# Kernel tuning notes

Measured on AMD Instinct MI355X. Metric: run time of the kernel, lower is better.

Reference implementation:

```python
import jax, jax.numpy as jnp
import numpy as np

DIM = 16      # latent_dim == sec
SEC = 16
SUB = 16      # sub_sec
E = SEC * SUB # num_elements = 256
TH = 0.2
BATCH = 128
SL = BATCH // 2
TAU = 0.0001

bexpm = jax.vmap(jax.scipy.linalg.expm)


def _commut(ge):
    # commutative(div=dim): loop over K=E//DIM block pairs with cumulative block
    # swaps; loss = sum_k cumsum(per-pair sq-diff)[k] / (DIM*E)^2
    K = E // DIM
    basis = ge.reshape(DIM, DIM * E)                 # [d, d*E]
    bm = jnp.matmul(ge, basis).reshape(DIM * E, DIM * E)
    R = bm[:K * DIM, :K * DIM].reshape(K, DIM, K, DIM)
    c = 2.0 * ((R - jnp.transpose(R, (2, 1, 0, 3))) ** 2).sum((1, 3))  # [K,K]
    iu, ju = np.triu_indices(K, k=1)                 # lexicographic pair order
    return jnp.cumsum(c[iu, ju]).sum() / float((DIM * E) ** 2)


def _independent(z, ge, sec_idx):
    B = z.shape[0]
    syms = bexpm(ge)                                 # [E,d,d]
    diff = z - jnp.matmul(z, syms)                   # [E,B,d]
    d2 = (diff ** 2).reshape(-1, DIM)
    sparse = jnp.mean((d2.sum(-1) - d2.max(-1)) ** 2)
    par = diff.reshape(SEC, SUB * B, DIM)            # [SEC,M,d]
    nrm = jnp.linalg.norm(par, axis=-1, keepdims=True)
    nn_ = jnp.einsum('smi,sni->smn', nrm, nrm)       # [SEC,M,M]
    dd = jnp.einsum('smd,snd->smn', par, par)
    parallel = jnp.mean(-jnp.log((dd / nn_) ** 2 + 1e-9))
    sel = diff.reshape(SEC, SUB, B, DIM)[jnp.arange(SEC), sec_idx]
    sel = sel.reshape(SEC * B, DIM)
    sn = jnp.linalg.norm(sel, axis=-1, keepdims=True)
    ratio = (sel @ sel.T) / (sn @ sn.T)
    mask = jnp.asarray(1.0 - np.kron(np.eye(SEC, dtype=np.float32),
                                     np.ones((B, B), np.float32)))
    orth = jnp.mean((ratio ** 2) * mask)
    return orth, parallel, _commut(ge), sparse


def reference(mean, logvar, latent_z, group_elements, lin_w, lin_b,
              gumbel_noise, sec_idx):
    B = latent_z.shape[0]
    sl = B // 2
    mean1, mean2 = mean[:sl], mean[sl:]
    std1 = jnp.exp(0.5 * logvar[:sl])
    std2 = jnp.exp(0.5 * mean[sl:])   # (faithful to source bug: uses mean)
    z1, z2 = latent_z[:sl], latent_z[sl:]
    orth, parallel, commut, sparse = _independent(latent_z, group_elements, sec_idx)

    zd = z1 - z2
    target = (jnp.abs(zd) > TH).astype(jnp.int32).reshape(-1)   # [sl*SEC]
    feat = jnp.concatenate([mean1, std1, mean2, std2], -1)       # [sl,4d]
    prob = feat @ lin_w.T + lin_b                                # [sl,18*SEC]
    sector_logits = prob[:, :2 * SEC].reshape(-1, 2)             # [sl*SEC,2]
    p = jax.nn.softmax(sector_logits, -1)
    ls = jax.nn.log_softmax(p, -1)    # cross_entropy applied to softmax output
    sector_loss = -jnp.take_along_axis(ls, target[:, None], 1).sum() / sl

    attn = jax.nn.softmax((sector_logits + gumbel_noise) / TAU, -1)
    switch = jnp.where((attn[:, 0] >= 0.5) | (attn[:, 1] > 0.5), attn[:, 1], 0.0)
    switch = switch.reshape(sl, SEC)
    fprob = jax.nn.softmax(prob[:, 2 * SEC:].reshape(sl, SEC, SUB), -1)
    fprob = fprob.reshape(sl, E)
    w = jnp.repeat(switch, SUB, axis=-1) * fprob                 # [sl,E]
    syms = w[:, :, None, None] * group_elements[None]            # [sl,E,d,d]
    sub_syms = syms.reshape(sl, SEC, SUB, DIM, DIM).sum(2)       # [sl,SEC,d,d]
    S = syms.sum(1)                                              # [sl,d,d]
    fwd_syms = bexpm(S)
    inv_syms = bexpm(-S)
    attn_score = jnp.concatenate([switch, fprob], -1)            # [sl,SEC+E]

    tz1 = jnp.einsum('bd,bde->be', z1, fwd_syms)
    tz2 = jnp.einsum('bd,bde->be', z2, inv_syms)
    equivariant = jnp.mean((tz2 - z1) ** 2) + jnp.mean((tz1 - z2) ** 2)
    return (tz1, tz2, fwd_syms, equivariant, attn_score,
            orth, parallel, commut, sparse, sector_loss, sub_syms)


def setup_inputs() -> dict:
    key = jax.random.key(0)
    ks = jax.random.split(key, 7)
    mean = jax.random.normal(ks[0], (BATCH, DIM), jnp.float32)
    logvar = jax.random.normal(ks[1], (BATCH, DIM), jnp.float32)
    latent_z = jax.random.normal(ks[2], (BATCH, DIM), jnp.float32)
    group_elements = 0.1 * jax.random.normal(ks[3], (E, DIM, DIM), jnp.float32)
    lin_w = 0.1 * jax.random.normal(ks[4], ((SUB + 2) * SEC, 4 * DIM), jnp.float32)
    lin_b = jnp.zeros(((SUB + 2) * SEC,), jnp.float32)
    u = jax.random.uniform(ks[5], (SL * SEC, 2), jnp.float32, 1e-6, 1.0 - 1e-6)
    gumbel_noise = -jnp.log(-jnp.log(u))
    sec_idx = jax.random.randint(ks[6], (SEC,), 0, SEC, jnp.int32)
    return {'mean': mean, 'logvar': logvar, 'latent_z': latent_z,
            'group_elements': group_elements, 'lin_w': lin_w, 'lin_b': lin_b,
            'gumbel_noise': gumbel_noise, 'sec_idx': sec_idx}
```

## Files before the change

kernel.cpp:

```cpp
#include <hip/hip_runtime.h>
#include <math.h>

#define O_TZ1      0
#define O_TZ2      1024
#define O_FWD      2048
#define O_EQUI     18432
#define O_ATTN     18433
#define O_ORTH     35841
#define O_PAR      35842
#define O_COMM     35843
#define O_SPARSE   35844
#define O_SECLOSS  35845
#define O_SUB      35846

#define P_SECLOSS  0
#define P_SPARSE   64
#define P_CPAIR    320
#define P_EQUI     440
#define P_PAR      504
#define P_ORTH     2680

typedef short s16x8 __attribute__((ext_vector_type(8)));
typedef float f32x4 __attribute__((ext_vector_type(4)));

__device__ __forceinline__ void block_store(float v, float* red, int t, float* slot, float scale)
{
    red[t] = v;
    __syncthreads();
    for (int off = 128; off > 0; off >>= 1) { if (t < off) red[t] += red[t+off]; __syncthreads(); }
    if (t == 0) *slot = red[0] * scale;
}

__device__ __forceinline__ unsigned short f2bf(float x)
{
    unsigned int u = __float_as_uint(x);
    u = (u + 0x7FFFu + ((u >> 16) & 1u)) >> 16;
    return (unsigned short)u;
}

__device__ __forceinline__ void expm_core(const float* __restrict__ src, float sign,
                                          float* sm, int* shi, int t)
{
    float* As = sm; float* T = sm + 256; float* P = sm + 512; float* rowsum = sm + 768;
    float a = src[t];
    As[t] = a;
    __syncthreads();
    if (t < 16) {
        float rs = 0.f;
        #pragma unroll
        for (int k = 0; k < 16; ++k) rs += fabsf(As[t*16+k]);
        rowsum[t] = rs;
    }
    __syncthreads();
    if (t == 0) {
        float nrm = 0.f;
        for (int i = 0; i < 16; ++i) nrm = fmaxf(nrm, rowsum[i]);
        int s = 0;
        if (nrm > 0.66f) { s = (int)ceilf(log2f(nrm * 1.51515f)); if (s < 0) s = 0; }
        *shi = s;
    }
    __syncthreads();
    int sq = *shi;
    float scale = sign * exp2f((float)(-sq));
    int i = t >> 4, j = t & 15;
    float as = a * scale;
    As[t] = as;
    T[t]  = ((i==j) ? 1.0f : 0.0f) + as;
    P[t]  = as;
    __syncthreads();
    for (int k = 2; k <= 8; ++k) {
        float accv = 0.f;
        #pragma unroll
        for (int m = 0; m < 16; ++m) accv += P[i*16+m]*As[m*16+j];
        float rk = 1.0f/(float)k;
        __syncthreads();
        float term = accv * rk;
        P[t] = term;
        T[t] += term;
        __syncthreads();
    }
    for (int q = 0; q < sq; ++q) {
        float accv = 0.f;
        #pragma unroll
        for (int m = 0; m < 16; ++m) accv += T[i*16+m]*T[m*16+j];
        __syncthreads();
        T[t] = accv;
        __syncthreads();
    }
}

template <bool DO_LOG>
__device__ __forceinline__ float gram_mfma(const unsigned short* __restrict__ diffb,
                                           int baseM, int baseN, int t)
{
    int lane = t & 63;
    int wave = t >> 6;
    int quad = lane >> 4;
    int col  = lane & 15;
    const s16x8* pb = (const s16x8*)diffb;
    s16x8 zf = {0,0,0,0,0,0,0,0};
    s16x8 A0 = zf, A1 = zf;
    s16x8 B0 = zf, B1 = zf, B2 = zf, B3 = zf, B4 = zf, B5 = zf, B6 = zf, B7 = zf;
    if (quad < 2) {
        int q = quad;
        A0 = pb[(baseM + wave*32      + col)*2 + q];
        A1 = pb[(baseM + wave*32 + 16 + col)*2 + q];
        B0 = pb[(baseN +   0 + col)*2 + q];
        B1 = pb[(baseN +  16 + col)*2 + q];
        B2 = pb[(baseN +  32 + col)*2 + q];
        B3 = pb[(baseN +  48 + col)*2 + q];
        B4 = pb[(baseN +  64 + col)*2 + q];
        B5 = pb[(baseN +  80 + col)*2 + q];
        B6 = pb[(baseN +  96 + col)*2 + q];
        B7 = pb[(baseN + 112 + col)*2 + q];
    }
    f32x4 cz = {0.f, 0.f, 0.f, 0.f};
    float accf = 0.f;
#define GTILE(AF, BF) { \
    f32x4 c = __builtin_amdgcn_mfma_f32_16x16x32_bf16(AF, BF, cz, 0, 0, 0); \
    _Pragma("unroll") \
    for (int r_ = 0; r_ < 4; ++r_) { \
        float v_ = c[r_]; \
        float x_ = v_*v_ + 1e-9f; \
        accf += DO_LOG ? __log2f(x_) : x_; \
    } }
    GTILE(A0,B0) GTILE(A0,B1) GTILE(A0,B2) GTILE(A0,B3)
    GTILE(A0,B4) GTILE(A0,B5) GTILE(A0,B6) GTILE(A0,B7)
    GTILE(A1,B0) GTILE(A1,B1) GTILE(A1,B2) GTILE(A1,B3)
    GTILE(A1,B4) GTILE(A1,B5) GTILE(A1,B6) GTILE(A1,B7)
#undef GTILE
    return accf;
}

__global__ void k_stage1(const float* __restrict__ mean, const float* __restrict__ logvar,
                         const float* __restrict__ latent, const float* __restrict__ ge,
                         const float* __restrict__ lin_w, const float* __restrict__ lin_b,
                         const float* __restrict__ gumbel,
                         float* __restrict__ out, float* __restrict__ S_ws,
                         unsigned short* __restrict__ diffb, float* __restrict__ part)
{
    __shared__ float smem[4864];
    __shared__ int shi;
    int bid = blockIdx.x;
    int t = threadIdx.x;

    if (bid < 64) {
        int b = bid;
        float* feat = smem;
        float* probb = smem + 64;
        float* red16 = smem + 352;
        float* wrow = smem + 368;
        if (t < 64) {
            int k = t; float v;
            if (k < 16)       v = mean[b*16 + k];
            else if (k < 32)  v = expf(0.5f * logvar[b*16 + (k-16)]);
            else if (k < 48)  v = mean[(64+b)*16 + (k-32)];
            else              v = expf(0.5f * mean[(64+b)*16 + (k-48)]);
            feat[k] = v;
        }
        __syncthreads();
        for (int j = t; j < 288; j += 256) {
            float a = lin_b[j];
            const float* wr = lin_w + j*64;
            #pragma unroll
            for (int k = 0; k < 64; ++k) a += feat[k]*wr[k];
            probb[j] = a;
        }
        __syncthreads();
        if (t < 16) {
            int s = t;
            float l0 = probb[2*s], l1 = probb[2*s+1];
            float M = fmaxf(l0,l1);
            float e0 = expf(l0-M), e1 = expf(l1-M);
            float Z = e0+e1;
            float p0 = e0/Z, p1 = e1/Z;
            float M2 = fmaxf(p0,p1);
            float lse = M2 + logf(expf(p0-M2)+expf(p1-M2));
            float ls0 = p0 - lse, ls1 = p1 - lse;
            float z1v = latent[b*16+s], z2v = latent[(64+b)*16+s];
            int tt = (fabsf(z1v - z2v) > 0.2f) ? 1 : 0;
            red16[s] = -(tt ? ls1 : ls0);
            int r = b*16 + s;
            float x0 = (l0 + gumbel[2*r])   * 10000.0f;
            float x1 = (l1 + gumbel[2*r+1]) * 10000.0f;
            float Ma = fmaxf(x0,x1);
            float a0 = expf(x0-Ma), a1 = expf(x1-Ma);
            float Za = a0+a1;
            a0 /= Za; a1 /= Za;
            float sw = ((a0 >= 0.5f) || (a1 > 0.5f)) ? a1 : 0.0f;
            out[O_ATTN + b*272 + s] = sw;
            const float* fl = &probb[32 + s*16];
            float mf = fl[0];
            #pragma unroll
            for (int u = 1; u < 16; ++u) mf = fmaxf(mf, fl[u]);
            float ex[16]; float Zf = 0.f;
            #pragma unroll
            for (int u = 0; u < 16; ++u) { ex[u] = expf(fl[u]-mf); Zf += ex[u]; }
            float rZ = 1.0f/Zf;
            #pragma unroll
            for (int u = 0; u < 16; ++u) {
                float fp = ex[u]*rZ;
                out[O_ATTN + b*272 + 16 + s*16 + u] = fp;
                wrow[s*16 + u] = sw*fp;
            }
        }
        __syncthreads();
        if (t == 0) {
            float s = 0.f;
            for (int i = 0; i < 16; ++i) s += red16[i];
            part[P_SECLOSS + b] = s;
        }
        float Stot = 0.f;
        for (int s = 0; s < 16; ++s) {
            float a = 0.f;
            #pragma unroll
            for (int u = 0; u < 16; ++u)
                a += wrow[s*16+u] * ge[(s*16+u)*256 + t];
            out[O_SUB + b*4096 + s*256 + t] = a;
            Stot += a;
        }
        S_ws[b*256 + t] = Stot;
    } else if (bid < 320) {
        int e = bid - 64;
        float* zsh = smem + 784;
        float* red = smem + 2832;
        #pragma unroll
        for (int q = 0; q < 8; ++q) zsh[t+256*q] = latent[t+256*q];
        expm_core(ge + e*256, 1.0f, smem, &shi, t);
        const float* T = smem + 256;
        float pv = 0.f;
        if (t < 128) {
            float zr[16];
            #pragma unroll
            for (int k = 0; k < 16; ++k) zr[k] = zsh[t*16+k];
            float dv[16];
            float sum = 0.f, mx = 0.f;
            #pragma unroll
            for (int d = 0; d < 16; ++d) {
                float a = 0.f;
                #pragma unroll
                for (int k = 0; k < 16; ++k) a += zr[k]*T[k*16+d];
                float v = zr[d] - a;
                dv[d] = v;
                float v2 = v*v;
                sum += v2; mx = fmaxf(mx, v2);
            }
            float sm2 = sum - mx;
            pv = sm2*sm2;
            float ri = 1.0f / sqrtf(sum);
            unsigned int pk[8];
            #pragma unroll
            for (int d = 0; d < 8; ++d) {
                unsigned short h0 = f2bf(dv[2*d]   * ri);
                unsigned short h1 = f2bf(dv[2*d+1] * ri);
                pk[d] = (unsigned int)h0 | ((unsigned int)h1 << 16);
            }
            uint4* dst = (uint4*)(diffb + (size_t)(e*128 + t)*16);
            dst[0] = make_uint4(pk[0], pk[1], pk[2], pk[3]);
            dst[1] = make_uint4(pk[4], pk[5], pk[6], pk[7]);
        }
        block_store(pv, red, t, part + P_SPARSE + e, 1.0f);
    } else {
        int idx = bid - 320;
        float* G = smem;
        float* gA = smem + 4096;
        float* gB = smem + 4352;
        float* red = smem + 4608;
        int a2 = 0, cnt = 15, rem = idx;
        while (rem >= cnt) { rem -= cnt; a2++; cnt--; }
        int b2 = a2 + 1 + rem;
        #pragma unroll
        for (int q = 0; q < 16; ++q) {
            int ii = t + 256*q;
            int k = ii >> 8, x = ii & 255;
            G[ii] = ge[k*16*256 + x];
        }
        gA[t] = ge[a2*256+t];
        gB[t] = ge[b2*256+t];
        __syncthreads();
        int i = t >> 4, j = t & 15;
        float v1 = 0.f, v2 = 0.f;
        #pragma unroll
        for (int k = 0; k < 16; ++k) {
            v1 += gA[i*16+k]*G[k*256 + b2*16 + j];
            v2 += gB[i*16+k]*G[k*256 + a2*16 + j];
        }
        float d = v1 - v2;
        block_store(d*d, red, t, part + P_CPAIR + idx, 2.0f);
    }
}

__global__ void __launch_bounds__(256) k_stage2(const float* __restrict__ latent,
                                                const float* __restrict__ S_ws,
                                                const unsigned short* __restrict__ diffb,
                                                const int* __restrict__ sec_idx,
                                                float* __restrict__ out,
                                                float* __restrict__ part)
{
    __shared__ float smem[1040];
    __shared__ int shi;
    int bid = blockIdx.x;
    int t = threadIdx.x;
    float* red = smem + 784;

    if (bid < 64) {
        int b = bid;
        expm_core(S_ws + b*256, 1.0f, smem, &shi, t);
        const float* T = smem + 256;
        out[O_FWD + b*256 + t] = T[t];
        float t1 = 0.f, z1d = 0.f, z2d = 0.f;
        if (t < 16) {
            int d = t;
            #pragma unroll
            for (int k = 0; k < 16; ++k) t1 += latent[b*16+k] * T[k*16+d];
            out[O_TZ1 + b*16 + d] = t1;
            z1d = latent[b*16+d];
            z2d = latent[(64+b)*16+d];
        }
        expm_core(S_ws + b*256, -1.0f, smem, &shi, t);
        float t2 = 0.f, ep = 0.f;
        if (t < 16) {
            int d = t;
            #pragma unroll
            for (int k = 0; k < 16; ++k) t2 += latent[(64+b)*16+k] * T[k*16+d];
            out[O_TZ2 + b*16 + d] = t2;
            ep = (t2 - z1d)*(t2 - z1d) + (t1 - z2d)*(t1 - z2d);
        }
        block_store(ep, red, t, part + P_EQUI + b, 1.0f);
    } else if (bid < 2240) {
        int tile = bid - 64;
        int s = tile & 15;
        int r = tile >> 4;
        int tm = 0;
        while (r >= 16 - tm) { r -= 16 - tm; tm++; }
        int tn = tm + r;
        float accf = gram_mfma<true>(diffb, s*2048 + tm*128, s*2048 + tn*128, t);
        float wt = (tm == tn) ? 1.0f : 2.0f;
        block_store(accf, red, t, part + P_PAR + tile, wt);
    } else {
        int idx = bid - 2240;
        int sm = 0, cnt = 15, rem = idx;
        while (rem >= cnt) { rem -= cnt; sm++; cnt--; }
        int sn = sm + 1 + rem;
        int em = sm*16 + sec_idx[sm];
        int en = sn*16 + sec_idx[sn];
        float accf = gram_mfma<false>(diffb, em*128, en*128, t);
        block_store(accf, red, t, part + P_ORTH + idx, 2.0f);
    }
}

__global__ void k_final(const float* __restrict__ part, float* __restrict__ out)
{
    __shared__ double dred[256];
    int t = threadIdx.x;

    double local = 0.0;
    for (int i = t; i < 2176; i += 256) local += (double)part[P_PAR + i];
    dred[t] = local;
    __syncthreads();
    for (int off = 128; off > 0; off >>= 1) { if (t < off) dred[t] += dred[t+off]; __syncthreads(); }
    double s_par = dred[0];
    __syncthreads();

    local = 0.0;
    if (t < 120) local += (double)part[P_ORTH + t];
    dred[t] = local;
    __syncthreads();
    for (int off = 128; off > 0; off >>= 1) { if (t < off) dred[t] += dred[t+off]; __syncthreads(); }
    double s_orth = dred[0];
    __syncthreads();

    local = 0.0;
    if (t < 64) local += (double)part[P_EQUI + t];
    if (t < 64) local += 0.0;
    dred[t] = local;
    __syncthreads();
    for (int off = 128; off > 0; off >>= 1) { if (t < off) dred[t] += dred[t+off]; __syncthreads(); }
    double s_equi = dred[0];
    __syncthreads();

    local = (t < 64) ? (double)part[P_SECLOSS + t] : 0.0;
    dred[t] = local;
    __syncthreads();
    for (int off = 128; off > 0; off >>= 1) { if (t < off) dred[t] += dred[t+off]; __syncthreads(); }
    double s_sec = dred[0];
    __syncthreads();

    dred[t] = (double)part[P_SPARSE + t];
    __syncthreads();
    for (int off = 128; off > 0; off >>= 1) { if (t < off) dred[t] += dred[t+off]; __syncthreads(); }
    double s_spa = dred[0];
    __syncthreads();

    local = 0.0;
    if (t < 120) local = (double)(120 - t) * (double)part[P_CPAIR + t];
    dred[t] = local;
    __syncthreads();
    for (int off = 128; off > 0; off >>= 1) { if (t < off) dred[t] += dred[t+off]; __syncthreads(); }

    if (t == 0) {
        out[O_COMM]    = (float)(dred[0] / 16777216.0);
        out[O_EQUI]    = (float)(s_equi / 1024.0);
        out[O_ORTH]    = (float)(s_orth / (2048.0*2048.0));
        out[O_PAR]     = (float)(-s_par * 0.6931471805599453 / 67108864.0);
        out[O_SPARSE]  = (float)(s_spa / 32768.0);
        out[O_SECLOSS] = (float)(s_sec / 64.0);
    }
}

extern "C" void kernel_launch(void* const* d_in, const int* in_sizes, int n_in,
                              void* d_out, int out_size, void* d_ws, size_t ws_size,
                              hipStream_t stream)
{
    const float* mean    = (const float*)d_in[0];
    const float* logvar  = (const float*)d_in[1];
    const float* latent  = (const float*)d_in[2];
    const float* ge      = (const float*)d_in[3];
    const float* lin_w   = (const float*)d_in[4];
    const float* lin_b   = (const float*)d_in[5];
    const float* gumbel  = (const float*)d_in[6];
    const int*   sec_idx = (const int*)d_in[7];
    float* out = (float*)d_out;

    char* ws = (char*)d_ws;
    float* part = (float*)ws;
    float* S_ws = (float*)(ws + 16384);
    unsigned short* diffb = (unsigned short*)(ws + 81920);

    k_stage1<<<440,  256, 0, stream>>>(mean, logvar, latent, ge, lin_w, lin_b, gumbel,
                                       out, S_ws, diffb, part);
    k_stage2<<<2360, 256, 0, stream>>>(latent, S_ws, diffb, sec_idx, out, part);
    k_final <<<1,    256, 0, stream>>>(part, out);
}
```

Baseline: 94.46 us.

## Fuse final reduction into stage2 via atomic accumulators and last-block finish

Removes the separate single-block final kernel. Stage2 blocks now add their partial sums into double-precision global accumulators with atomics and bump an arrival counter, and the last block to arrive computes and writes the scalar losses. The log-sum in the gram tiles is also restructured to multiply four terms and take one log2 instead of four. This saves a kernel launch and its serialization at the cost of atomics on contended addresses. The product-then-log form could lose precision or underflow when values are tiny.

```diff
diff --git a/kernel.cpp b/kernel.cpp
--- a/kernel.cpp
+++ b/kernel.cpp
@@ -16,9 +16,8 @@
 #define P_SECLOSS  0
 #define P_SPARSE   64
 #define P_CPAIR    320
-#define P_EQUI     440
-#define P_PAR      504
-#define P_ORTH     2680
+
+#define S2_BLOCKS  2360u
 
 typedef short s16x8 __attribute__((ext_vector_type(8)));
 typedef float f32x4 __attribute__((ext_vector_type(4)));
@@ -29,6 +28,22 @@
     __syncthreads();
     for (int off = 128; off > 0; off >>= 1) { if (t < off) red[t] += red[t+off]; __syncthreads(); }
     if (t == 0) *slot = red[0] * scale;
+}
+
+__device__ __forceinline__ bool block_arrive(float v, float* red, int t, double* dst, float scale,
+                                             unsigned int* counter, unsigned int* lf)
+{
+    red[t] = v;
+    __syncthreads();
+    for (int off = 128; off > 0; off >>= 1) { if (t < off) red[t] += red[t+off]; __syncthreads(); }
+    if (t == 0) {
+        double oldv = atomicAdd(dst, (double)(red[0] * scale));
+        float dep = (float)oldv;
+        __asm__ volatile("" : : "v"(dep));
+        *lf = (atomicAdd(counter, 1u) == S2_BLOCKS - 1u) ? 1u : 0u;
+    }
+    __syncthreads();
+    return *lf != 0u;
 }
 
 __device__ __forceinline__ unsigned short f2bf(float x)
@@ -118,11 +133,12 @@
     float accf = 0.f;
 #define GTILE(AF, BF) { \
     f32x4 c = __builtin_amdgcn_mfma_f32_16x16x32_bf16(AF, BF, cz, 0, 0, 0); \
-    _Pragma("unroll") \
-    for (int r_ = 0; r_ < 4; ++r_) { \
-        float v_ = c[r_]; \
-        float x_ = v_*v_ + 1e-9f; \
-        accf += DO_LOG ? __log2f(x_) : x_; \
+    if (DO_LOG) { \
+        float p0 = (c[0]*c[0] + 1e-9f) * (c[1]*c[1] + 1e-9f); \
+        float p1 = (c[2]*c[2] + 1e-9f) * (c[3]*c[3] + 1e-9f); \
+        accf += __log2f(p0 * p1); \
+    } else { \
+        accf += c[0]*c[0] + c[1]*c[1] + c[2]*c[2] + c[3]*c[3]; \
     } }
     GTILE(A0,B0) GTILE(A0,B1) GTILE(A0,B2) GTILE(A0,B3)
     GTILE(A0,B4) GTILE(A0,B5) GTILE(A0,B6) GTILE(A0,B7)
@@ -132,17 +148,35 @@
     return accf;
 }
 
+__device__ __forceinline__ double dsum(const float* __restrict__ p, int n, int t, double* dred)
+{
+    double local = 0.0;
+    for (int i = t; i < n; i += 256) local += (double)p[i];
+    dred[t] = local;
+    __syncthreads();
+    for (int off = 128; off > 0; off >>= 1) { if (t < off) dred[t] += dred[t+off]; __syncthreads(); }
+    double r = dred[0];
+    __syncthreads();
+    return r;
+}
+
 __global__ void k_stage1(const float* __restrict__ mean, const float* __restrict__ logvar,
                          const float* __restrict__ latent, const float* __restrict__ ge,
                          const float* __restrict__ lin_w, const float* __restrict__ lin_b,
                          const float* __restrict__ gumbel,
                          float* __restrict__ out, float* __restrict__ S_ws,
-                         unsigned short* __restrict__ diffb, float* __restrict__ part)
+                         unsigned short* __restrict__ diffb, float* __restrict__ part,
+                         double* __restrict__ acc, unsigned int* __restrict__ counter)
 {
     __shared__ float smem[4864];
     __shared__ int shi;
     int bid = blockIdx.x;
     int t = threadIdx.x;
+
+    if (bid == 0 && t == 0) {
+        acc[0] = 0.0; acc[1] = 0.0; acc[2] = 0.0;
+        *counter = 0u;
+    }
 
     if (bid < 64) {
         int b = bid;
@@ -295,13 +329,19 @@
                                                 const unsigned short* __restrict__ diffb,
                                                 const int* __restrict__ sec_idx,
                                                 float* __restrict__ out,
-                                                float* __restrict__ part)
+                                                float* __restrict__ part,
+                                                double* __restrict__ acc,
+                                                unsigned int* __restrict__ counter)
 {
     __shared__ float smem[1040];
+    __shared__ double dred[256];
+    __shared__ double sacc[3];
     __shared__ int shi;
+    __shared__ unsigned int lf;
     int bid = blockIdx.x;
     int t = threadIdx.x;
     float* red = smem + 784;
+    bool last;
 
     if (bid < 64) {
         int b = bid;
@@ -326,7 +366,7 @@
             out[O_TZ2 + b*16 + d] = t2;
             ep = (t2 - z1d)*(t2 - z1d) + (t1 - z2d)*(t1 - z2d);
         }
-        block_store(ep, red, t, part + P_EQUI + b, 1.0f);
+        last = block_arrive(ep, red, t, &acc[2], 1.0f, counter, &lf);
     } else if (bid < 2240) {
         int tile = bid - 64;
         int s = tile & 15;
@@ -336,7 +376,7 @@
         int tn = tm + r;
         float accf = gram_mfma<true>(diffb, s*2048 + tm*128, s*2048 + tn*128, t);
         float wt = (tm == tn) ? 1.0f : 2.0f;
-        block_store(accf, red, t, part + P_PAR + tile, wt);
+        last = block_arrive(accf, red, t, &acc[0], wt, counter, &lf);
     } else {
         int idx = bid - 2240;
         int sm = 0, cnt = 15, rem = idx;
@@ -345,66 +385,31 @@
         int em = sm*16 + sec_idx[sm];
         int en = sn*16 + sec_idx[sn];
         float accf = gram_mfma<false>(diffb, em*128, en*128, t);
-        block_store(accf, red, t, part + P_ORTH + idx, 2.0f);
-    }
-}
-
-__global__ void k_final(const float* __restrict__ part, float* __restrict__ out)
-{
-    __shared__ double dred[256];
-    int t = threadIdx.x;
-
-    double local = 0.0;
-    for (int i = t; i < 2176; i += 256) local += (double)part[P_PAR + i];
-    dred[t] = local;
-    __syncthreads();
-    for (int off = 128; off > 0; off >>= 1) { if (t < off) dred[t] += dred[t+off]; __syncthreads(); }
-    double s_par = dred[0];
-    __syncthreads();
-
-    local = 0.0;
-    if (t < 120) local += (double)part[P_ORTH + t];
-    dred[t] = local;
-    __syncthreads();
-    for (int off = 128; off > 0; off >>= 1) { if (t < off) dred[t] += dred[t+off]; __syncthreads(); }
-    double s_orth = dred[0];
-    __syncthreads();
-
-    local = 0.0;
-    if (t < 64) local += (double)part[P_EQUI + t];
-    if (t < 64) local += 0.0;
-    dred[t] = local;
-    __syncthreads();
-    for (int off = 128; off > 0; off >>= 1) { if (t < off) dred[t] += dred[t+off]; __syncthreads(); }
-    double s_equi = dred[0];
-    __syncthreads();
-
-    local = (t < 64) ? (double)part[P_SECLOSS + t] : 0.0;
-    dred[t] = local;
-    __syncthreads();
-    for (int off = 128; off > 0; off >>= 1) { if (t < off) dred[t] += dred[t+off]; __syncthreads(); }
-    double s_sec = dred[0];
-    __syncthreads();
-
-    dred[t] = (double)part[P_SPARSE + t];
-    __syncthreads();
-    for (int off = 128; off > 0; off >>= 1) { if (t < off) dred[t] += dred[t+off]; __syncthreads(); }
-    double s_spa = dred[0];
-    __syncthreads();
-
-    local = 0.0;
-    if (t < 120) local = (double)(120 - t) * (double)part[P_CPAIR + t];
-    dred[t] = local;
-    __syncthreads();
-    for (int off = 128; off > 0; off >>= 1) { if (t < off) dred[t] += dred[t+off]; __syncthreads(); }
-
-    if (t == 0) {
-        out[O_COMM]    = (float)(dred[0] / 16777216.0);
-        out[O_EQUI]    = (float)(s_equi / 1024.0);
-        out[O_ORTH]    = (float)(s_orth / (2048.0*2048.0));
-        out[O_PAR]     = (float)(-s_par * 0.6931471805599453 / 67108864.0);
-        out[O_SPARSE]  = (float)(s_spa / 32768.0);
-        out[O_SECLOSS] = (float)(s_sec / 64.0);
+        last = block_arrive(accf, red, t, &acc[1], 2.0f, counter, &lf);
+    }
+
+    if (last) {
+        if (t == 0) {
+            sacc[0] = atomicAdd(&acc[0], 0.0);
+            sacc[1] = atomicAdd(&acc[1], 0.0);
+            sacc[2] = atomicAdd(&acc[2], 0.0);
+        }
+        __syncthreads();
+        double s_sec = dsum(part + P_SECLOSS, 64, t, dred);
+        double s_spa = dsum(part + P_SPARSE, 256, t, dred);
+        double local = 0.0;
+        if (t < 120) local = (double)(120 - t) * (double)part[P_CPAIR + t];
+        dred[t] = local;
+        __syncthreads();
+        for (int off = 128; off > 0; off >>= 1) { if (t < off) dred[t] += dred[t+off]; __syncthreads(); }
+        if (t == 0) {
+            out[O_COMM]    = (float)(dred[0] / 16777216.0);
+            out[O_EQUI]    = (float)(sacc[2] / 1024.0);
+            out[O_ORTH]    = (float)(sacc[1] / (2048.0*2048.0));
+            out[O_PAR]     = (float)(-sacc[0] * 0.6931471805599453 / 67108864.0);
+            out[O_SPARSE]  = (float)(s_spa / 32768.0);
+            out[O_SECLOSS] = (float)(s_sec / 64.0);
+        }
     }
 }
 
@@ -423,12 +428,13 @@
     float* out = (float*)d_out;
 
     char* ws = (char*)d_ws;
-    float* part = (float*)ws;
+    double* acc = (double*)ws;
+    float* part = (float*)(ws + 64);
+    unsigned int* counter = (unsigned int*)(ws + 12288);
     float* S_ws = (float*)(ws + 16384);
     unsigned short* diffb = (unsigned short*)(ws + 81920);
 
     k_stage1<<<440,  256, 0, stream>>>(mean, logvar, latent, ge, lin_w, lin_b, gumbel,
-                                       out, S_ws, diffb, part);
-    k_stage2<<<2360, 256, 0, stream>>>(latent, S_ws, diffb, sec_idx, out, part);
-    k_final <<<1,    256, 0, stream>>>(part, out);
-}
+                                       out, S_ws, diffb, part, acc, counter);
+    k_stage2<<<2360, 256, 0, stream>>>(latent, S_ws, diffb, sec_idx, out, part, acc, counter);
+}
```

Result: slower. 117.2 us (+24.1%).

## Stage gram tiles through LDS, batch log2 calls, use wave-shuffle reductions

Applied to the files above, without the earlier changes.

The gram-tile blocks in stage2 now copy their 128+128 bf16 rows into padded shared memory with coalesced 16-byte loads. MFMA operands are then read from LDS instead of issuing scattered global loads per wave. The log-sum now multiplies four squared terms before one log2, cutting transcendental count, at some risk of underflow or precision loss in the product. The block reduction is replaced with wave shuffles plus a 4-entry LDS combine, removing the 8-step barrier tree.

```diff
diff --git a/kernel.cpp b/kernel.cpp
--- a/kernel.cpp
+++ b/kernel.cpp
@@ -31,6 +31,15 @@
     if (t == 0) *slot = red[0] * scale;
 }
 
+__device__ __forceinline__ void block_store2(float v, float* red4, int t, float* slot, float scale)
+{
+    #pragma unroll
+    for (int off = 32; off > 0; off >>= 1) v += __shfl_down(v, off);
+    if ((t & 63) == 0) red4[t >> 6] = v;
+    __syncthreads();
+    if (t == 0) *slot = (red4[0] + red4[1] + red4[2] + red4[3]) * scale;
+}
+
 __device__ __forceinline__ unsigned short f2bf(float x)
 {
     unsigned int u = __float_as_uint(x);
@@ -90,39 +99,46 @@
 }
 
 template <bool DO_LOG>
-__device__ __forceinline__ float gram_mfma(const unsigned short* __restrict__ diffb,
-                                           int baseM, int baseN, int t)
-{
-    int lane = t & 63;
-    int wave = t >> 6;
-    int quad = lane >> 4;
-    int col  = lane & 15;
-    const s16x8* pb = (const s16x8*)diffb;
+__device__ __forceinline__ float gram_tile_lds(const unsigned short* __restrict__ diffb,
+                                               short* tiles, int baseM, int baseN, int t)
+{
+    const uint4* gd = (const uint4*)diffb;
+    #pragma unroll
+    for (int q = 0; q < 2; ++q) {
+        int idx = t + 256*q;
+        int row = idx >> 1, half = idx & 1;
+        int grow = (row < 128) ? (baseM + row) : (baseN + (row - 128));
+        uint4 v = gd[grow*2 + half];
+        *(uint4*)(tiles + row*24 + half*8) = v;
+    }
+    __syncthreads();
+    int lane = t & 63, wave = t >> 6, quad = lane >> 4, col = lane & 15;
     s16x8 zf = {0,0,0,0,0,0,0,0};
-    s16x8 A0 = zf, A1 = zf;
-    s16x8 B0 = zf, B1 = zf, B2 = zf, B3 = zf, B4 = zf, B5 = zf, B6 = zf, B7 = zf;
+    s16x8 A0=zf, A1=zf, B0=zf, B1=zf, B2=zf, B3=zf, B4=zf, B5=zf, B6=zf, B7=zf;
     if (quad < 2) {
-        int q = quad;
-        A0 = pb[(baseM + wave*32      + col)*2 + q];
-        A1 = pb[(baseM + wave*32 + 16 + col)*2 + q];
-        B0 = pb[(baseN +   0 + col)*2 + q];
-        B1 = pb[(baseN +  16 + col)*2 + q];
-        B2 = pb[(baseN +  32 + col)*2 + q];
-        B3 = pb[(baseN +  48 + col)*2 + q];
-        B4 = pb[(baseN +  64 + col)*2 + q];
-        B5 = pb[(baseN +  80 + col)*2 + q];
-        B6 = pb[(baseN +  96 + col)*2 + q];
-        B7 = pb[(baseN + 112 + col)*2 + q];
+        const short* tm_ = tiles;
+        const short* tn_ = tiles + 128*24;
+        A0 = *(const s16x8*)(tm_ + (wave*32      + col)*24 + quad*8);
+        A1 = *(const s16x8*)(tm_ + (wave*32 + 16 + col)*24 + quad*8);
+        B0 = *(const s16x8*)(tn_ + (  0 + col)*24 + quad*8);
+        B1 = *(const s16x8*)(tn_ + ( 16 + col)*24 + quad*8);
+        B2 = *(const s16x8*)(tn_ + ( 32 + col)*24 + quad*8);
+        B3 = *(const s16x8*)(tn_ + ( 48 + col)*24 + quad*8);
+        B4 = *(const s16x8*)(tn_ + ( 64 + col)*24 + quad*8);
+        B5 = *(const s16x8*)(tn_ + ( 80 + col)*24 + quad*8);
+        B6 = *(const s16x8*)(tn_ + ( 96 + col)*24 + quad*8);
+        B7 = *(const s16x8*)(tn_ + (112 + col)*24 + quad*8);
     }
     f32x4 cz = {0.f, 0.f, 0.f, 0.f};
     float accf = 0.f;
 #define GTILE(AF, BF) { \
     f32x4 c = __builtin_amdgcn_mfma_f32_16x16x32_bf16(AF, BF, cz, 0, 0, 0); \
-    _Pragma("unroll") \
-    for (int r_ = 0; r_ < 4; ++r_) { \
-        float v_ = c[r_]; \
-        float x_ = v_*v_ + 1e-9f; \
-        accf += DO_LOG ? __log2f(x_) : x_; \
+    if (DO_LOG) { \
+        float p0 = (c[0]*c[0] + 1e-9f) * (c[1]*c[1] + 1e-9f); \
+        float p1 = (c[2]*c[2] + 1e-9f) * (c[3]*c[3] + 1e-9f); \
+        accf += __log2f(p0 * p1); \
+    } else { \
+        accf += c[0]*c[0] + c[1]*c[1] + c[2]*c[2] + c[3]*c[3]; \
     } }
     GTILE(A0,B0) GTILE(A0,B1) GTILE(A0,B2) GTILE(A0,B3)
     GTILE(A0,B4) GTILE(A0,B5) GTILE(A0,B6) GTILE(A0,B7)
@@ -297,11 +313,11 @@
                                                 float* __restrict__ out,
                                                 float* __restrict__ part)
 {
-    __shared__ float smem[1040];
+    __shared__ float smem[3328];
     __shared__ int shi;
     int bid = blockIdx.x;
     int t = threadIdx.x;
-    float* red = smem + 784;
+    float* red4 = smem + 3072;
 
     if (bid < 64) {
         int b = bid;
@@ -326,7 +342,7 @@
             out[O_TZ2 + b*16 + d] = t2;
             ep = (t2 - z1d)*(t2 - z1d) + (t1 - z2d)*(t1 - z2d);
         }
-        block_store(ep, red, t, part + P_EQUI + b, 1.0f);
+        block_store2(ep, red4, t, part + P_EQUI + b, 1.0f);
     } else if (bid < 2240) {
         int tile = bid - 64;
         int s = tile & 15;
@@ -334,9 +350,9 @@
         int tm = 0;
         while (r >= 16 - tm) { r -= 16 - tm; tm++; }
         int tn = tm + r;
-        float accf = gram_mfma<true>(diffb, s*2048 + tm*128, s*2048 + tn*128, t);
+        float accf = gram_tile_lds<true>(diffb, (short*)smem, s*2048 + tm*128, s*2048 + tn*128, t);
         float wt = (tm == tn) ? 1.0f : 2.0f;
-        block_store(accf, red, t, part + P_PAR + tile, wt);
+        block_store2(accf, red4, t, part + P_PAR + tile, wt);
     } else {
         int idx = bid - 2240;
         int sm = 0, cnt = 15, rem = idx;
@@ -344,8 +360,8 @@
         int sn = sm + 1 + rem;
         int em = sm*16 + sec_idx[sm];
         int en = sn*16 + sec_idx[sn];
-        float accf = gram_mfma<false>(diffb, em*128, en*128, t);
-        block_store(accf, red, t, part + P_ORTH + idx, 2.0f);
+        float accf = gram_tile_lds<false>(diffb, (short*)smem, em*128, en*128, t);
+        block_store2(accf, red4, t, part + P_ORTH + idx, 2.0f);
     }
 }
 
@@ -372,7 +388,6 @@
 
     local = 0.0;
     if (t < 64) local += (double)part[P_EQUI + t];
-    if (t < 64) local += 0.0;
     dred[t] = local;
     __syncthreads();
     for (int off = 128; off > 0; off >>= 1) { if (t < off) dred[t] += dred[t+off]; __syncthreads(); }
```

Result: no change. 92.98 us (-1.6%).
